# Kernel tuning notes

Hardware: AMD Instinct MI355X
Metric: run time of the kernel (lower is better)

## Reference

```python
import jax, jax.numpy as jnp
import numpy as np

DIM, H, DH = 1024, 16, 64
SCALE = 1.0 / np.sqrt(DH)


def setup_inputs() -> dict:
    key = jax.random.key(0)
    ks = jax.random.split(key, 16)
    B, S = 2, 2048
    glorot = jax.nn.initializers.glorot_uniform()
    def qkv(k):
        return glorot(k, (DIM, H, DH), jnp.float32)
    inp = {
        "x": jax.random.normal(ks[0], (B, S, DIM), jnp.float32),
        "layer_idx": 3,
        "lambda_param": jnp.full((1,), 0.8, jnp.float32),
    }
    for i, br in enumerate(["1", "2"]):
        base = 1 + i * 4
        inp[f"Wq{br}"] = qkv(ks[base])
        inp[f"Wk{br}"] = qkv(ks[base + 1])
        inp[f"Wv{br}"] = qkv(ks[base + 2])
        inp[f"Wo{br}"] = glorot(ks[base + 3], (H, DH, DIM), jnp.float32).reshape(H, DH, DIM)
        inp[f"bq{br}"] = jnp.zeros((H, DH), jnp.float32)
        inp[f"bk{br}"] = jnp.zeros((H, DH), jnp.float32)
        inp[f"bv{br}"] = jnp.zeros((H, DH), jnp.float32)
        inp[f"bo{br}"] = jnp.zeros((DIM,), jnp.float32)
    inp["Wp"] = glorot(ks[9], (DIM, DIM), jnp.float32)
    inp["bp"] = jnp.zeros((DIM,), jnp.float32)
    return inp


def _mha(x, Wq, bq, Wk, bk, Wv, bv, Wo, bo):
    # x: [B,S,D]; per-head projections as in keras.layers.MultiHeadAttention
    q = jnp.einsum("bsd,dhk->bshk", x, Wq) + bq   # [B,S,H,Dh]
    k = jnp.einsum("bsd,dhk->bshk", x, Wk) + bk
    v = jnp.einsum("bsd,dhk->bshk", x, Wv) + bv
    scores = jnp.einsum("bqhd,bkhd->bhqk", q, k) * SCALE  # [B,H,S,S]
    attn = jax.nn.softmax(scores, axis=-1)
    o = jnp.einsum("bhqk,bkhd->bqhd", attn, v)            # [B,S,H,Dh]
    return jnp.einsum("bqhd,hdo->bqo", o, Wo) + bo        # [B,S,D]


def _get_lambda(lambda_param, layer_idx):
    lf = jnp.asarray(layer_idx, jnp.float32)
    exp_term = jnp.exp(-0.3 * jnp.maximum(lf - 1.0, 0.0))
    init = 0.8 - 0.6 * exp_term
    return jnp.clip(init * lambda_param[0], 0.1, 0.9)


def reference(x, layer_idx, lambda_param,
              Wq1, bq1, Wk1, bk1, Wv1, bv1, Wo1, bo1,
              Wq2, bq2, Wk2, bk2, Wv2, bv2, Wo2, bo2,
              Wp, bp):
    a1 = _mha(x, Wq1, bq1, Wk1, bk1, Wv1, bv1, Wo1, bo1)
    a2 = _mha(x, Wq2, bq2, Wk2, bk2, Wv2, bv2, Wo2, bo2)
    lam = _get_lambda(lambda_param, layer_idx)
    diff = a1 - lam * a2
    return diff @ Wp + bp  # dropout is identity at inference
```

## Files before the change

kernel.cpp:

```cpp
#include <hip/hip_runtime.h>
#include <math.h>

typedef unsigned short u16;
typedef __attribute__((ext_vector_type(8))) short bf16x8;
typedef __attribute__((ext_vector_type(4))) float f32x4;
typedef __attribute__((ext_vector_type(4))) unsigned short u16x4;
typedef __attribute__((ext_vector_type(8))) unsigned short u16x8;

constexpr int Sq = 2048, Dm = 1024, Hh = 16, DH = 64;
constexpr int NT = 4096;
constexpr float SEXP = 0.125f * 1.44269504f;

#if __has_builtin(__builtin_amdgcn_exp2f)
#define EXP2(x) __builtin_amdgcn_exp2f(x)
#else
#define EXP2(x) exp2f(x)
#endif

__device__ __forceinline__ u16 f2bf(float f) {
    unsigned u = __float_as_uint(f);
    return (u16)((u + 0x7FFF + ((u >> 16) & 1)) >> 16);
}

__device__ __forceinline__ void async16(u16* lds, const u16* g) {
    __builtin_amdgcn_global_load_lds(
        (const __attribute__((address_space(1))) unsigned int*)g,
        (__attribute__((address_space(3))) unsigned int*)lds, 16, 0, 0);
}

__device__ __forceinline__ float lam_of(const int* lidx, const float* lamp) {
    float lf = (float)lidx[0];
    float init = 0.8f - 0.6f * __expf(-0.3f * fmaxf(lf - 1.0f, 0.0f));
    return fminf(fmaxf(init * lamp[0], 0.1f), 0.9f);
}

__device__ __forceinline__ void gemm_tile_128(
    const u16* __restrict__ A, const u16* __restrict__ Bt, int K,
    int aRow0, int bCol0, u16* As, u16* Bs, f32x4 acc[4][4])
{
    const int tid = threadIdx.x;
    const int w = tid >> 6, lane = tid & 63;
    const int ln = lane & 15, quad = lane >> 4;
    const int wm = (w >> 1) * 64, wn = (w & 1) * 64;
    const int l3 = lane & 7, lr8 = lane >> 3;

    for (int kt = 0; kt < K; kt += 64) {
        __syncthreads();
        #pragma unroll
        for (int c0 = 0; c0 < 4; ++c0) {
            int c = w * 4 + c0;
            int lr = c * 8 + lr8;
            int sc = l3 ^ (lr & 7);
            async16(As + c * 512, A + (size_t)(aRow0 + lr) * K + kt + sc * 8);
            async16(Bs + c * 512, Bt + (size_t)(bCol0 + lr) * K + kt + sc * 8);
        }
        __syncthreads();
        #pragma unroll
        for (int kc = 0; kc < 2; ++kc) {
            bf16x8 af[4], bfr[4];
            #pragma unroll
            for (int mt = 0; mt < 4; ++mt)
                af[mt] = *(const bf16x8*)(As + (wm + mt * 16 + ln) * 64 +
                                          (((kc * 4 + quad) ^ (ln & 7)) * 8));
            #pragma unroll
            for (int nt = 0; nt < 4; ++nt)
                bfr[nt] = *(const bf16x8*)(Bs + (wn + nt * 16 + ln) * 64 +
                                           (((kc * 4 + quad) ^ (ln & 7)) * 8));
            #pragma unroll
            for (int mt = 0; mt < 4; ++mt)
                #pragma unroll
                for (int nt = 0; nt < 4; ++nt)
                    acc[mt][nt] = __builtin_amdgcn_mfma_f32_16x16x32_bf16(
                        af[mt], bfr[nt], acc[mt][nt], 0, 0, 0);
        }
    }
}

__device__ __forceinline__ void gemm_tile_64(
    const u16* __restrict__ A, const u16* __restrict__ Bt, int K,
    int aRow0, int bCol0, u16* As, u16* Bs, f32x4 acc[2][4])
{
    const int tid = threadIdx.x;
    const int w = tid >> 6, lane = tid & 63;
    const int ln = lane & 15, quad = lane >> 4;
    const int wm = (w >> 1) * 32, wn = (w & 1) * 64;
    const int l3 = lane & 7, lr8 = lane >> 3;

    for (int kt = 0; kt < K; kt += 64) {
        __syncthreads();
        #pragma unroll
        for (int c0 = 0; c0 < 2; ++c0) {
            int c = w * 2 + c0;
            int lr = c * 8 + lr8;
            int sc = l3 ^ (lr & 7);
            async16(As + c * 512, A + (size_t)(aRow0 + lr) * K + kt + sc * 8);
        }
        #pragma unroll
        for (int c0 = 0; c0 < 4; ++c0) {
            int c = w * 4 + c0;
            int lr = c * 8 + lr8;
            int sc = l3 ^ (lr & 7);
            async16(Bs + c * 512, Bt + (size_t)(bCol0 + lr) * K + kt + sc * 8);
        }
        __syncthreads();
        #pragma unroll
        for (int kc = 0; kc < 2; ++kc) {
            bf16x8 af[2], bfr[4];
            #pragma unroll
            for (int mt = 0; mt < 2; ++mt)
                af[mt] = *(const bf16x8*)(As + (wm + mt * 16 + ln) * 64 +
                                          (((kc * 4 + quad) ^ (ln & 7)) * 8));
            #pragma unroll
            for (int nt = 0; nt < 4; ++nt)
                bfr[nt] = *(const bf16x8*)(Bs + (wn + nt * 16 + ln) * 64 +
                                           (((kc * 4 + quad) ^ (ln & 7)) * 8));
            #pragma unroll
            for (int mt = 0; mt < 2; ++mt)
                #pragma unroll
                for (int nt = 0; nt < 4; ++nt)
                    acc[mt][nt] = __builtin_amdgcn_mfma_f32_16x16x32_bf16(
                        af[mt], bfr[nt], acc[mt][nt], 0, 0, 0);
        }
    }
}

__global__ __launch_bounds__(256)
void convert_x(const float* __restrict__ x, u16* __restrict__ xb)
{
    int i = (blockIdx.x * 256 + threadIdx.x) * 4;
    float4 v = *(const float4*)(x + i);
    u16x4 o;
    o.x = f2bf(v.x); o.y = f2bf(v.y); o.z = f2bf(v.z); o.w = f2bf(v.w);
    *(u16x4*)(xb + i) = o;
}

struct TcP { const float* src[7]; u16* dst[7]; };

__global__ __launch_bounds__(256)
void wconv(TcP p)
{
    __shared__ float t[64][65];
    const int z = blockIdx.z;
    const float* __restrict__ src = p.src[z];
    u16* __restrict__ dst = p.dst[z];
    const int kb = blockIdx.y * 64, nb = blockIdx.x * 64;
    const int tid = threadIdx.x;
    {
        int r = tid >> 2, cs = (tid & 3) * 16;
        #pragma unroll
        for (int j4 = 0; j4 < 16; j4 += 4) {
            float4 v = *(const float4*)&src[(size_t)(kb + r) * 1024 + nb + cs + j4];
            t[r][cs + j4 + 0] = v.x; t[r][cs + j4 + 1] = v.y;
            t[r][cs + j4 + 2] = v.z; t[r][cs + j4 + 3] = v.w;
        }
    }
    __syncthreads();
    {
        int n = tid >> 2, ks = (tid & 3) * 16;
        u16x8 a, b;
        #pragma unroll
        for (int j = 0; j < 8; ++j) a[j] = f2bf(t[ks + j][n]);
        #pragma unroll
        for (int j = 0; j < 8; ++j) b[j] = f2bf(t[ks + 8 + j][n]);
        u16* o = &dst[(size_t)(nb + n) * 1024 + kb + ks];
        *(u16x8*)o = a;
        *(u16x8*)(o + 8) = b;
    }
}

__global__ __launch_bounds__(256)
void woconv(const float* __restrict__ Wo1, const float* __restrict__ Wo2,
            const float* __restrict__ bo1, const float* __restrict__ bo2,
            const int* __restrict__ lidx, const float* __restrict__ lamp,
            u16* __restrict__ Acat)
{
    const float lam = lam_of(lidx, lamp);
    int i = (blockIdx.x * 256 + threadIdx.x) * 4;
    float4 v;
    if (i < 1048576) {
        v = *(const float4*)(Wo1 + i);
    } else if (i < 2097152) {
        v = *(const float4*)(Wo2 + (i - 1048576));
        v.x *= -lam; v.y *= -lam; v.z *= -lam; v.w *= -lam;
    } else {
        int c = i - 2097152;
        float4 a = *(const float4*)(bo1 + c);
        float4 b = *(const float4*)(bo2 + c);
        v.x = a.x - lam * b.x; v.y = a.y - lam * b.y;
        v.z = a.z - lam * b.z; v.w = a.w - lam * b.w;
    }
    u16x4 o;
    o.x = f2bf(v.x); o.y = f2bf(v.y); o.z = f2bf(v.z); o.w = f2bf(v.w);
    *(u16x4*)(Acat + i) = o;
}

__global__ __launch_bounds__(256, 4)
void wfull_mfma(const u16* __restrict__ Acat, const u16* __restrict__ Wpt,
                const float* __restrict__ bp, u16* __restrict__ Wfull_bt,
                float* __restrict__ bfull)
{
    __shared__ u16 As[64 * 64], Bs[128 * 64];
    const int aRow0 = blockIdx.y * 64, nCol0 = blockIdx.x * 128;
    f32x4 acc[2][4] = {};
    gemm_tile_64(Acat, Wpt, 1024, aRow0, nCol0, As, Bs, acc);

    const int tid = threadIdx.x, w = tid >> 6, lane = tid & 63;
    const int ln = lane & 15, quad = lane >> 4;
    const int wm = (w >> 1) * 32, wn = (w & 1) * 64;
    #pragma unroll
    for (int mt = 0; mt < 2; ++mt) {
        #pragma unroll
        for (int nt = 0; nt < 4; ++nt) {
            int gn = nCol0 + wn + nt * 16 + ln;
            #pragma unroll
            for (int r = 0; r < 4; ++r) {
                int gm = aRow0 + wm + mt * 16 + quad * 4 + r;
                if (gm < 2048)
                    Wfull_bt[(size_t)gn * 2048 + gm] = f2bf(acc[mt][nt][r]);
                else if (gm == 2048)
                    bfull[gn] = acc[mt][nt][r] + bp[gn];
            }
        }
    }
}

struct QkvP { const u16* Wt[6]; const float* bias[6]; u16* out[6]; };

__global__ __launch_bounds__(256, 3)
void qkv_mfma(const u16* __restrict__ xb, QkvP p)
{
    __shared__ u16 As[128 * 64], Bs[128 * 64];
    const int z = blockIdx.z;
    const int type = (z < 3) ? z : z - 3;
    const int aRow0 = blockIdx.y * 128, nCol0 = blockIdx.x * 128;
    f32x4 acc[4][4] = {};
    gemm_tile_128(xb, p.Wt[z], 1024, aRow0, nCol0, As, Bs, acc);

    const float* __restrict__ bias = p.bias[z];
    u16* __restrict__ out = p.out[z];
    const int tid = threadIdx.x, w = tid >> 6, lane = tid & 63;
    const int ln = lane & 15, quad = lane >> 4;
    const int wm = (w >> 1) * 64, wn = (w & 1) * 64;
    #pragma unroll
    for (int mt = 0; mt < 4; ++mt) {
        #pragma unroll
        for (int nt = 0; nt < 4; ++nt) {
            int gn = nCol0 + wn + nt * 16 + ln;
            int h = gn >> 6, dh = gn & 63;
            float bv = bias[gn];
            #pragma unroll
            for (int r = 0; r < 4; ++r) {
                int gm = aRow0 + wm + mt * 16 + quad * 4 + r;
                int b = gm >> 11, s = gm & (Sq - 1);
                size_t bh = (size_t)(b * Hh + h);
                float fv = acc[mt][nt][r] + bv;
                size_t idx;
                u16 val;
                if (type == 0) {
                    val = f2bf(fv * SEXP);
                    idx = bh * 131072 + (size_t)s * 64 + dh;
                } else if (type == 1) {
                    val = f2bf(fv);
                    idx = bh * 131072 + (size_t)(s >> 5) * 2048 +
                          (size_t)((dh >> 5) * 2 + ((s >> 4) & 1)) * 512 +
                          (size_t)(((dh >> 3) & 3) * 16 + (s & 15)) * 8 + (dh & 7);
                } else {
                    val = f2bf(fv);
                    int kidx = ((s & 15) * 2) + ((s >> 4) & 1);
                    idx = bh * 131072 + (size_t)(s >> 5) * 2048 +
                          (size_t)(dh >> 4) * 512 +
                          (size_t)((kidx >> 3) * 16 + (dh & 15)) * 8 + (kidx & 7);
                }
                out[idx] = val;
            }
        }
    }
}

__global__ __launch_bounds__(256, 4)
void attn_mfma(const u16* __restrict__ q1, const u16* __restrict__ kf1,
               const u16* __restrict__ vf1,
               const u16* __restrict__ q2, const u16* __restrict__ kf2,
               const u16* __restrict__ vf2, u16* __restrict__ ocat)
{
    __shared__ __align__(16) char smem[10240];

    const int bh = blockIdx.x, qblk = blockIdx.y, br = blockIdx.z;
    const u16* __restrict__ q  = br ? q2  : q1;
    const u16* __restrict__ kf = br ? kf2 : kf1;
    const u16* __restrict__ vf = br ? vf2 : vf1;

    const int tid = threadIdx.x, w = tid >> 6, lane = tid & 63;
    const int ln = lane & 15, quad = lane >> 4;
    char* Pbase = smem + w * 2560;

    const u16* qbase = q + (size_t)bh * 131072 +
                       (size_t)(qblk * 128 + w * 32) * 64;
    bf16x8 qf[2][2];
    #pragma unroll
    for (int mt = 0; mt < 2; ++mt)
        #pragma unroll
        for (int kc = 0; kc < 2; ++kc)
            qf[mt][kc] = *(const bf16x8*)(qbase + (mt * 16 + ln) * 64 +
                                          kc * 32 + quad * 8);

    bf16x8 ones;
    #pragma unroll
    for (int j = 0; j < 8; ++j) ones[j] = (short)0x3F80;
    const f32x4 zero4 = {0.f, 0.f, 0.f, 0.f};

    f32x4 oacc[2][4] = {};
    f32x4 lacc[2] = {};

    const u16* kbase = kf + (size_t)bh * 131072 + lane * 8;
    const u16* vbase = vf + (size_t)bh * 131072 + lane * 8;

    for (int it = 0; it < 32; ++it) {
        #pragma unroll
        for (int u = 0; u < 2; ++u) {
            const int kt = it * 2 + u;
            const u16* kp = kbase + (size_t)kt * 2048;
            const u16* vp = vbase + (size_t)kt * 2048;

            bf16x8 kfr[2][2];
            #pragma unroll
            for (int kc = 0; kc < 2; ++kc)
                #pragma unroll
                for (int nt = 0; nt < 2; ++nt)
                    kfr[nt][kc] = *(const bf16x8*)(kp + (kc * 2 + nt) * 512);

            f32x4 sacc[2][2];
            #pragma unroll
            for (int mt = 0; mt < 2; ++mt)
                #pragma unroll
                for (int nt = 0; nt < 2; ++nt)
                    sacc[mt][nt] = __builtin_amdgcn_mfma_f32_16x16x32_bf16(
                        qf[mt][0], kfr[nt][0], zero4, 0, 0, 0);
            #pragma unroll
            for (int mt = 0; mt < 2; ++mt)
                #pragma unroll
                for (int nt = 0; nt < 2; ++nt)
                    sacc[mt][nt] = __builtin_amdgcn_mfma_f32_16x16x32_bf16(
                        qf[mt][1], kfr[nt][1], sacc[mt][nt], 0, 0, 0);

            #pragma unroll
            for (int mt = 0; mt < 2; ++mt) {
                #pragma unroll
                for (int r = 0; r < 4; ++r) {
                    float p0 = EXP2(sacc[mt][0][r]);
                    float p1 = EXP2(sacc[mt][1][r]);
                    unsigned a  = __float_as_uint(p0) + 0x8000u;
                    unsigned b2 = __float_as_uint(p1) + 0x8000u;
                    unsigned pk = __builtin_amdgcn_perm(b2, a, 0x07060302);
                    int row = mt * 16 + quad * 4 + r;
                    *(unsigned*)(Pbase + row * 80 + (((ln >> 2) ^ r) << 4) +
                                 ((ln & 3) << 2)) = pk;
                }
            }

            bf16x8 vfr[4];
            #pragma unroll
            for (int dt = 0; dt < 4; ++dt)
                vfr[dt] = *(const bf16x8*)(vp + dt * 512);

            #pragma unroll
            for (int mt = 0; mt < 2; ++mt) {
                bf16x8 pf = *(const bf16x8*)(Pbase + (mt * 16 + ln) * 80 +
                                             ((quad ^ (ln & 3)) << 4));
                lacc[mt] = __builtin_amdgcn_mfma_f32_16x16x32_bf16(
                    pf, ones, lacc[mt], 0, 0, 0);
                #pragma unroll
                for (int dt = 0; dt < 4; ++dt)
                    oacc[mt][dt] = __builtin_amdgcn_mfma_f32_16x16x32_bf16(
                        pf, vfr[dt], oacc[mt][dt], 0, 0, 0);
            }
        }
        __builtin_amdgcn_s_barrier();
    }

    const int b = bh >> 4, h = bh & 15;
    #pragma unroll
    for (int mt = 0; mt < 2; ++mt) {
        #pragma unroll
        for (int r = 0; r < 4; ++r) {
            float inv = 1.0f / lacc[mt][r];
            int s = qblk * 128 + w * 32 + mt * 16 + quad * 4 + r;
            size_t rowb = (size_t)(b * Sq + s) * 2048 + br * 1024 + h * 64;
            #pragma unroll
            for (int dt = 0; dt < 4; ++dt)
                ocat[rowb + dt * 16 + ln] = f2bf(oacc[mt][dt][r] * inv);
        }
    }
}

__global__ __launch_bounds__(256, 4)
void out_mfma(const u16* __restrict__ ocat, const u16* __restrict__ Wfull_bt,
              const float* __restrict__ bfull, float* __restrict__ outb)
{
    __shared__ u16 As[64 * 64], Bs[128 * 64];
    const int aRow0 = blockIdx.y * 64, nCol0 = blockIdx.x * 128;
    f32x4 acc[2][4] = {};
    gemm_tile_64(ocat, Wfull_bt, 2048, aRow0, nCol0, As, Bs, acc);

    const int tid = threadIdx.x, w = tid >> 6, lane = tid & 63;
    const int ln = lane & 15, quad = lane >> 4;
    const int wm = (w >> 1) * 32, wn = (w & 1) * 64;
    #pragma unroll
    for (int mt = 0; mt < 2; ++mt) {
        #pragma unroll
        for (int nt = 0; nt < 4; ++nt) {
            int gn = nCol0 + wn + nt * 16 + ln;
            float bv = bfull[gn];
            #pragma unroll
            for (int r = 0; r < 4; ++r) {
                int gm = aRow0 + wm + mt * 16 + quad * 4 + r;
                outb[(size_t)gm * 1024 + gn] = acc[mt][nt][r] + bv;
            }
        }
    }
}

extern "C" void kernel_launch(void* const* d_in, const int* in_sizes, int n_in,
                              void* d_out, int out_size, void* d_ws, size_t ws_size,
                              hipStream_t stream)
{
    const float* x    = (const float*)d_in[0];
    const int*   lidx = (const int*)  d_in[1];
    const float* lamp = (const float*)d_in[2];
    const float* Wq1  = (const float*)d_in[3];
    const float* Wk1  = (const float*)d_in[4];
    const float* Wv1  = (const float*)d_in[5];
    const float* Wo1  = (const float*)d_in[6];
    const float* bq1  = (const float*)d_in[7];
    const float* bk1  = (const float*)d_in[8];
    const float* bv1  = (const float*)d_in[9];
    const float* bo1  = (const float*)d_in[10];
    const float* Wq2  = (const float*)d_in[11];
    const float* Wk2  = (const float*)d_in[12];
    const float* Wv2  = (const float*)d_in[13];
    const float* Wo2  = (const float*)d_in[14];
    const float* bq2  = (const float*)d_in[15];
    const float* bk2  = (const float*)d_in[16];
    const float* bv2  = (const float*)d_in[17];
    const float* bo2  = (const float*)d_in[18];
    const float* Wp   = (const float*)d_in[19];
    const float* bp   = (const float*)d_in[20];

    char* wsb = (char*)d_ws;
    const size_t MB = 1 << 20;
    u16* xb    = (u16*)(wsb + 0 * MB);
    u16* Wt0   = (u16*)(wsb + 8 * MB);
    u16* Wpt   = (u16*)(wsb + 20 * MB);
    u16* Acat  = (u16*)(wsb + 22 * MB);
    u16* Wfull = (u16*)(wsb + 27 * MB);
    float* bfull = (float*)(wsb + 31 * MB);
    u16* qb1   = (u16*)(wsb + 32 * MB);
    u16* kb1   = (u16*)(wsb + 40 * MB);
    u16* vb1   = (u16*)(wsb + 48 * MB);
    u16* qb2   = (u16*)(wsb + 56 * MB);
    u16* kb2   = (u16*)(wsb + 64 * MB);
    u16* vb2   = (u16*)(wsb + 72 * MB);
    u16* ocat  = (u16*)(wsb + 80 * MB);

    convert_x<<<dim3(NT * Dm / 1024), dim3(256), 0, stream>>>(x, xb);

    TcP tp;
    const float* wsrc[7] = {Wq1, Wk1, Wv1, Wq2, Wk2, Wv2, Wp};
    for (int i = 0; i < 7; ++i) tp.src[i] = wsrc[i];
    for (int i = 0; i < 6; ++i) tp.dst[i] = Wt0 + (size_t)i * 1024 * 1024;
    tp.dst[6] = Wpt;
    wconv<<<dim3(16, 16, 7), dim3(256), 0, stream>>>(tp);

    woconv<<<dim3(2049), dim3(256), 0, stream>>>(
        Wo1, Wo2, bo1, bo2, lidx, lamp, Acat);

    wfull_mfma<<<dim3(8, 33), dim3(256), 0, stream>>>(
        Acat, Wpt, bp, Wfull, bfull);

    QkvP qp;
    qp.Wt[0] = Wt0 + 0 * 1048576; qp.bias[0] = bq1; qp.out[0] = qb1;
    qp.Wt[1] = Wt0 + 1 * 1048576; qp.bias[1] = bk1; qp.out[1] = kb1;
    qp.Wt[2] = Wt0 + 2 * 1048576; qp.bias[2] = bv1; qp.out[2] = vb1;
    qp.Wt[3] = Wt0 + 3 * 1048576; qp.bias[3] = bq2; qp.out[3] = qb2;
    qp.Wt[4] = Wt0 + 4 * 1048576; qp.bias[4] = bk2; qp.out[4] = kb2;
    qp.Wt[5] = Wt0 + 5 * 1048576; qp.bias[5] = bv2; qp.out[5] = vb2;
    qkv_mfma<<<dim3(8, 32, 6), dim3(256), 0, stream>>>(xb, qp);

    attn_mfma<<<dim3(32, 16, 2), dim3(256), 0, stream>>>(
        qb1, kb1, vb1, qb2, kb2, vb2, ocat);

    out_mfma<<<dim3(8, 64), dim3(256), 0, stream>>>(
        ocat, Wfull, bfull, (float*)d_out);
}
```

Measured before the change: 333.2 us.

## Widen QKV GEMM tiles to 128x256 and software-pipeline attention P buffer

The QKV projection now treats the six weight matrices as one concatenated 6144-wide B operand and uses 128x256 tiles, so each wave holds 4x8 accumulators. This halves redundant A-tile loads, at the cost of more registers and occupancy lowered to 2. The attention loop now double-buffers the per-wave P tile in LDS and software-pipelines QK^T/exp for key tile k with the PV product for tile k-1. This overlaps exp work with MFMA, but doubles LDS use and lowers the occupancy hint from 4 to 3.

```diff
diff --git a/kernel.cpp b/kernel.cpp
--- a/kernel.cpp
+++ b/kernel.cpp
@@ -32,48 +32,6 @@
     float lf = (float)lidx[0];
     float init = 0.8f - 0.6f * __expf(-0.3f * fmaxf(lf - 1.0f, 0.0f));
     return fminf(fmaxf(init * lamp[0], 0.1f), 0.9f);
-}
-
-__device__ __forceinline__ void gemm_tile_128(
-    const u16* __restrict__ A, const u16* __restrict__ Bt, int K,
-    int aRow0, int bCol0, u16* As, u16* Bs, f32x4 acc[4][4])
-{
-    const int tid = threadIdx.x;
-    const int w = tid >> 6, lane = tid & 63;
-    const int ln = lane & 15, quad = lane >> 4;
-    const int wm = (w >> 1) * 64, wn = (w & 1) * 64;
-    const int l3 = lane & 7, lr8 = lane >> 3;
-
-    for (int kt = 0; kt < K; kt += 64) {
-        __syncthreads();
-        #pragma unroll
-        for (int c0 = 0; c0 < 4; ++c0) {
-            int c = w * 4 + c0;
-            int lr = c * 8 + lr8;
-            int sc = l3 ^ (lr & 7);
-            async16(As + c * 512, A + (size_t)(aRow0 + lr) * K + kt + sc * 8);
-            async16(Bs + c * 512, Bt + (size_t)(bCol0 + lr) * K + kt + sc * 8);
-        }
-        __syncthreads();
-        #pragma unroll
-        for (int kc = 0; kc < 2; ++kc) {
-            bf16x8 af[4], bfr[4];
-            #pragma unroll
-            for (int mt = 0; mt < 4; ++mt)
-                af[mt] = *(const bf16x8*)(As + (wm + mt * 16 + ln) * 64 +
-                                          (((kc * 4 + quad) ^ (ln & 7)) * 8));
-            #pragma unroll
-            for (int nt = 0; nt < 4; ++nt)
-                bfr[nt] = *(const bf16x8*)(Bs + (wn + nt * 16 + ln) * 64 +
-                                           (((kc * 4 + quad) ^ (ln & 7)) * 8));
-            #pragma unroll
-            for (int mt = 0; mt < 4; ++mt)
-                #pragma unroll
-                for (int nt = 0; nt < 4; ++nt)
-                    acc[mt][nt] = __builtin_amdgcn_mfma_f32_16x16x32_bf16(
-                        af[mt], bfr[nt], acc[mt][nt], 0, 0, 0);
-        }
-    }
 }
 
 __device__ __forceinline__ void gemm_tile_64(
@@ -224,30 +182,71 @@
     }
 }
 
-struct QkvP { const u16* Wt[6]; const float* bias[6]; u16* out[6]; };
-
-__global__ __launch_bounds__(256, 3)
-void qkv_mfma(const u16* __restrict__ xb, QkvP p)
-{
-    __shared__ u16 As[128 * 64], Bs[128 * 64];
-    const int z = blockIdx.z;
+struct QkvP { const float* bias[6]; u16* out[6]; };
+
+__global__ __launch_bounds__(256, 2)
+void qkv_mfma(const u16* __restrict__ xb, const u16* __restrict__ Wt_all, QkvP p)
+{
+    __shared__ u16 As[128 * 64], Bs[256 * 64];
+    const int nCol0 = blockIdx.x * 256;
+    const int aRow0 = blockIdx.y * 128;
+    const int z = nCol0 >> 10;
     const int type = (z < 3) ? z : z - 3;
-    const int aRow0 = blockIdx.y * 128, nCol0 = blockIdx.x * 128;
-    f32x4 acc[4][4] = {};
-    gemm_tile_128(xb, p.Wt[z], 1024, aRow0, nCol0, As, Bs, acc);
+
+    const int tid = threadIdx.x, w = tid >> 6, lane = tid & 63;
+    const int ln = lane & 15, quad = lane >> 4;
+    const int wm = (w >> 1) * 64, wn = (w & 1) * 128;
+    const int l3 = lane & 7, lr8 = lane >> 3;
+
+    f32x4 acc[4][8] = {};
+
+    for (int kt = 0; kt < 1024; kt += 64) {
+        __syncthreads();
+        #pragma unroll
+        for (int c0 = 0; c0 < 4; ++c0) {
+            int c = w * 4 + c0;
+            int lr = c * 8 + lr8;
+            int sc = l3 ^ (lr & 7);
+            async16(As + c * 512, xb + (size_t)(aRow0 + lr) * 1024 + kt + sc * 8);
+        }
+        #pragma unroll
+        for (int c0 = 0; c0 < 8; ++c0) {
+            int c = w * 8 + c0;
+            int lr = c * 8 + lr8;
+            int sc = l3 ^ (lr & 7);
+            async16(Bs + c * 512,
+                    Wt_all + (size_t)(nCol0 + lr) * 1024 + kt + sc * 8);
+        }
+        __syncthreads();
+        #pragma unroll
+        for (int kc = 0; kc < 2; ++kc) {
+            bf16x8 af[4], bfr[8];
+            #pragma unroll
+            for (int mt = 0; mt < 4; ++mt)
+                af[mt] = *(const bf16x8*)(As + (wm + mt * 16 + ln) * 64 +
+                                          (((kc * 4 + quad) ^ (ln & 7)) * 8));
+            #pragma unroll
+            for (int nt = 0; nt < 8; ++nt)
+                bfr[nt] = *(const bf16x8*)(Bs + (wn + nt * 16 + ln) * 64 +
+                                           (((kc * 4 + quad) ^ (ln & 7)) * 8));
+            #pragma unroll
+            for (int mt = 0; mt < 4; ++mt)
+                #pragma unroll
+                for (int nt = 0; nt < 8; ++nt)
+                    acc[mt][nt] = __builtin_amdgcn_mfma_f32_16x16x32_bf16(
+                        af[mt], bfr[nt], acc[mt][nt], 0, 0, 0);
+        }
+    }
 
     const float* __restrict__ bias = p.bias[z];
     u16* __restrict__ out = p.out[z];
-    const int tid = threadIdx.x, w = tid >> 6, lane = tid & 63;
-    const int ln = lane & 15, quad = lane >> 4;
-    const int wm = (w >> 1) * 64, wn = (w & 1) * 64;
     #pragma unroll
     for (int mt = 0; mt < 4; ++mt) {
         #pragma unroll
-        for (int nt = 0; nt < 4; ++nt) {
-            int gn = nCol0 + wn + nt * 16 + ln;
-            int h = gn >> 6, dh = gn & 63;
-            float bv = bias[gn];
+        for (int nt = 0; nt < 8; ++nt) {
+            int col = (nCol0 + wn + nt * 16 + ln) & 1023;
+            int h = col >> 6, dh = col & 63;
+            float bv = bias[col];
             #pragma unroll
             for (int r = 0; r < 4; ++r) {
                 int gm = aRow0 + wm + mt * 16 + quad * 4 + r;
@@ -277,13 +276,74 @@
     }
 }
 
-__global__ __launch_bounds__(256, 4)
+__device__ __forceinline__ void attn_step(
+    int kt, const u16* kbase, const u16* vbase, char* Pw, char* Pr,
+    const bf16x8 qf[2][2], bf16x8 ones,
+    f32x4 oacc[2][4], f32x4 lacc[2], int ln, int quad)
+{
+    const f32x4 zero4 = {0.f, 0.f, 0.f, 0.f};
+    const u16* kp = kbase + (size_t)kt * 2048;
+    const u16* vp = vbase + (size_t)(kt - 1) * 2048;
+
+    bf16x8 kfr[2][2], vfr[4];
+    #pragma unroll
+    for (int kc = 0; kc < 2; ++kc)
+        #pragma unroll
+        for (int nt = 0; nt < 2; ++nt)
+            kfr[nt][kc] = *(const bf16x8*)(kp + (kc * 2 + nt) * 512);
+    #pragma unroll
+    for (int dt = 0; dt < 4; ++dt)
+        vfr[dt] = *(const bf16x8*)(vp + dt * 512);
+
+    f32x4 sacc[2][2];
+    #pragma unroll
+    for (int mt = 0; mt < 2; ++mt)
+        #pragma unroll
+        for (int nt = 0; nt < 2; ++nt)
+            sacc[mt][nt] = __builtin_amdgcn_mfma_f32_16x16x32_bf16(
+                qf[mt][0], kfr[nt][0], zero4, 0, 0, 0);
+    #pragma unroll
+    for (int mt = 0; mt < 2; ++mt)
+        #pragma unroll
+        for (int nt = 0; nt < 2; ++nt)
+            sacc[mt][nt] = __builtin_amdgcn_mfma_f32_16x16x32_bf16(
+                qf[mt][1], kfr[nt][1], sacc[mt][nt], 0, 0, 0);
+
+    #pragma unroll
+    for (int mt = 0; mt < 2; ++mt) {
+        #pragma unroll
+        for (int r = 0; r < 4; ++r) {
+            float p0 = EXP2(sacc[mt][0][r]);
+            float p1 = EXP2(sacc[mt][1][r]);
+            unsigned a  = __float_as_uint(p0) + 0x8000u;
+            unsigned b2 = __float_as_uint(p1) + 0x8000u;
+            unsigned pk = __builtin_amdgcn_perm(b2, a, 0x07060302);
+            int row = mt * 16 + quad * 4 + r;
+            *(unsigned*)(Pw + row * 80 + (((ln >> 2) ^ r) << 4) +
+                         ((ln & 3) << 2)) = pk;
+        }
+    }
+
+    #pragma unroll
+    for (int mt = 0; mt < 2; ++mt) {
+        bf16x8 pf = *(const bf16x8*)(Pr + (mt * 16 + ln) * 80 +
+                                     ((quad ^ (ln & 3)) << 4));
+        lacc[mt] = __builtin_amdgcn_mfma_f32_16x16x32_bf16(
+            pf, ones, lacc[mt], 0, 0, 0);
+        #pragma unroll
+        for (int dt = 0; dt < 4; ++dt)
+            oacc[mt][dt] = __builtin_amdgcn_mfma_f32_16x16x32_bf16(
+                pf, vfr[dt], oacc[mt][dt], 0, 0, 0);
+    }
+}
+
+__global__ __launch_bounds__(256, 3)
 void attn_mfma(const u16* __restrict__ q1, const u16* __restrict__ kf1,
                const u16* __restrict__ vf1,
                const u16* __restrict__ q2, const u16* __restrict__ kf2,
                const u16* __restrict__ vf2, u16* __restrict__ ocat)
 {
-    __shared__ __align__(16) char smem[10240];
+    __shared__ __align__(16) char smem[20480];
 
     const int bh = blockIdx.x, qblk = blockIdx.y, br = blockIdx.z;
     const u16* __restrict__ q  = br ? q2  : q1;
@@ -292,7 +352,8 @@
 
     const int tid = threadIdx.x, w = tid >> 6, lane = tid & 63;
     const int ln = lane & 15, quad = lane >> 4;
-    char* Pbase = smem + w * 2560;
+    char* P0 = smem + w * 5120;
+    char* P1 = P0 + 2560;
 
     const u16* qbase = q + (size_t)bh * 131072 +
                        (size_t)(qblk * 128 + w * 32) * 64;
@@ -315,67 +376,66 @@
     const u16* kbase = kf + (size_t)bh * 131072 + lane * 8;
     const u16* vbase = vf + (size_t)bh * 131072 + lane * 8;
 
-    for (int it = 0; it < 32; ++it) {
-        #pragma unroll
-        for (int u = 0; u < 2; ++u) {
-            const int kt = it * 2 + u;
-            const u16* kp = kbase + (size_t)kt * 2048;
-            const u16* vp = vbase + (size_t)kt * 2048;
-
-            bf16x8 kfr[2][2];
-            #pragma unroll
-            for (int kc = 0; kc < 2; ++kc)
-                #pragma unroll
-                for (int nt = 0; nt < 2; ++nt)
-                    kfr[nt][kc] = *(const bf16x8*)(kp + (kc * 2 + nt) * 512);
-
-            f32x4 sacc[2][2];
-            #pragma unroll
-            for (int mt = 0; mt < 2; ++mt)
-                #pragma unroll
-                for (int nt = 0; nt < 2; ++nt)
-                    sacc[mt][nt] = __builtin_amdgcn_mfma_f32_16x16x32_bf16(
-                        qf[mt][0], kfr[nt][0], zero4, 0, 0, 0);
-            #pragma unroll
-            for (int mt = 0; mt < 2; ++mt)
-                #pragma unroll
-                for (int nt = 0; nt < 2; ++nt)
-                    sacc[mt][nt] = __builtin_amdgcn_mfma_f32_16x16x32_bf16(
-                        qf[mt][1], kfr[nt][1], sacc[mt][nt], 0, 0, 0);
-
-            #pragma unroll
-            for (int mt = 0; mt < 2; ++mt) {
-                #pragma unroll
-                for (int r = 0; r < 4; ++r) {
-                    float p0 = EXP2(sacc[mt][0][r]);
-                    float p1 = EXP2(sacc[mt][1][r]);
-                    unsigned a  = __float_as_uint(p0) + 0x8000u;
-                    unsigned b2 = __float_as_uint(p1) + 0x8000u;
-                    unsigned pk = __builtin_amdgcn_perm(b2, a, 0x07060302);
-                    int row = mt * 16 + quad * 4 + r;
-                    *(unsigned*)(Pbase + row * 80 + (((ln >> 2) ^ r) << 4) +
-                                 ((ln & 3) << 2)) = pk;
-                }
+    {
+        bf16x8 kfr[2][2];
+        #pragma unroll
+        for (int kc = 0; kc < 2; ++kc)
+            #pragma unroll
+            for (int nt = 0; nt < 2; ++nt)
+                kfr[nt][kc] = *(const bf16x8*)(kbase + (kc * 2 + nt) * 512);
+        f32x4 sacc[2][2];
+        #pragma unroll
+        for (int mt = 0; mt < 2; ++mt)
+            #pragma unroll
+            for (int nt = 0; nt < 2; ++nt)
+                sacc[mt][nt] = __builtin_amdgcn_mfma_f32_16x16x32_bf16(
+                    qf[mt][0], kfr[nt][0], zero4, 0, 0, 0);
+        #pragma unroll
+        for (int mt = 0; mt < 2; ++mt)
+            #pragma unroll
+            for (int nt = 0; nt < 2; ++nt)
+                sacc[mt][nt] = __builtin_amdgcn_mfma_f32_16x16x32_bf16(
+                    qf[mt][1], kfr[nt][1], sacc[mt][nt], 0, 0, 0);
+        #pragma unroll
+        for (int mt = 0; mt < 2; ++mt) {
+            #pragma unroll
+            for (int r = 0; r < 4; ++r) {
+                float p0 = EXP2(sacc[mt][0][r]);
+                float p1 = EXP2(sacc[mt][1][r]);
+                unsigned a  = __float_as_uint(p0) + 0x8000u;
+                unsigned b2 = __float_as_uint(p1) + 0x8000u;
+                unsigned pk = __builtin_amdgcn_perm(b2, a, 0x07060302);
+                int row = mt * 16 + quad * 4 + r;
+                *(unsigned*)(P0 + row * 80 + (((ln >> 2) ^ r) << 4) +
+                             ((ln & 3) << 2)) = pk;
             }
-
-            bf16x8 vfr[4];
+        }
+    }
+
+    for (int it = 0; it < 31; ++it) {
+        attn_step(2 * it + 1, kbase, vbase, P1, P0, qf, ones, oacc, lacc, ln, quad);
+        attn_step(2 * it + 2, kbase, vbase, P0, P1, qf, ones, oacc, lacc, ln, quad);
+        __builtin_amdgcn_s_barrier();
+    }
+    attn_step(63, kbase, vbase, P1, P0, qf, ones, oacc, lacc, ln, quad);
+
+    {
+        const u16* vp = vbase + (size_t)63 * 2048;
+        bf16x8 vfr[4];
+        #pragma unroll
+        for (int dt = 0; dt < 4; ++dt)
+            vfr[dt] = *(const bf16x8*)(vp + dt * 512);
+        #pragma unroll
+        for (int mt = 0; mt < 2; ++mt) {
+            bf16x8 pf = *(const bf16x8*)(P1 + (mt * 16 + ln) * 80 +
+                                         ((quad ^ (ln & 3)) << 4));
+            lacc[mt] = __builtin_amdgcn_mfma_f32_16x16x32_bf16(
+                pf, ones, lacc[mt], 0, 0, 0);
             #pragma unroll
             for (int dt = 0; dt < 4; ++dt)
-                vfr[dt] = *(const bf16x8*)(vp + dt * 512);
-
-            #pragma unroll
-            for (int mt = 0; mt < 2; ++mt) {
-                bf16x8 pf = *(const bf16x8*)(Pbase + (mt * 16 + ln) * 80 +
-                                             ((quad ^ (ln & 3)) << 4));
-                lacc[mt] = __builtin_amdgcn_mfma_f32_16x16x32_bf16(
-                    pf, ones, lacc[mt], 0, 0, 0);
-                #pragma unroll
-                for (int dt = 0; dt < 4; ++dt)
-                    oacc[mt][dt] = __builtin_amdgcn_mfma_f32_16x16x32_bf16(
-                        pf, vfr[dt], oacc[mt][dt], 0, 0, 0);
-            }
-        }
-        __builtin_amdgcn_s_barrier();
+                oacc[mt][dt] = __builtin_amdgcn_mfma_f32_16x16x32_bf16(
+                    pf, vfr[dt], oacc[mt][dt], 0, 0, 0);
+        }
     }
 
     const int b = bh >> 4, h = bh & 15;
@@ -467,7 +527,7 @@
     TcP tp;
     const float* wsrc[7] = {Wq1, Wk1, Wv1, Wq2, Wk2, Wv2, Wp};
     for (int i = 0; i < 7; ++i) tp.src[i] = wsrc[i];
-    for (int i = 0; i < 6; ++i) tp.dst[i] = Wt0 + (size_t)i * 1024 * 1024;
+    for (int i = 0; i < 6; ++i) tp.dst[i] = Wt0 + (size_t)i * 1048576;
     tp.dst[6] = Wpt;
     wconv<<<dim3(16, 16, 7), dim3(256), 0, stream>>>(tp);
 
@@ -478,13 +538,13 @@
         Acat, Wpt, bp, Wfull, bfull);
 
     QkvP qp;
-    qp.Wt[0] = Wt0 + 0 * 1048576; qp.bias[0] = bq1; qp.out[0] = qb1;
-    qp.Wt[1] = Wt0 + 1 * 1048576; qp.bias[1] = bk1; qp.out[1] = kb1;
-    qp.Wt[2] = Wt0 + 2 * 1048576; qp.bias[2] = bv1; qp.out[2] = vb1;
-    qp.Wt[3] = Wt0 + 3 * 1048576; qp.bias[3] = bq2; qp.out[3] = qb2;
-    qp.Wt[4] = Wt0 + 4 * 1048576; qp.bias[4] = bk2; qp.out[4] = kb2;
-    qp.Wt[5] = Wt0 + 5 * 1048576; qp.bias[5] = bv2; qp.out[5] = vb2;
-    qkv_mfma<<<dim3(8, 32, 6), dim3(256), 0, stream>>>(xb, qp);
+    qp.bias[0] = bq1; qp.out[0] = qb1;
+    qp.bias[1] = bk1; qp.out[1] = kb1;
+    qp.bias[2] = bv1; qp.out[2] = vb1;
+    qp.bias[3] = bq2; qp.out[3] = qb2;
+    qp.bias[4] = bk2; qp.out[4] = kb2;
+    qp.bias[5] = bv2; qp.out[5] = vb2;
+    qkv_mfma<<<dim3(24, 32), dim3(256), 0, stream>>>(xb, Wt0, qp);
 
     attn_mfma<<<dim3(32, 16, 2), dim3(256), 0, stream>>>(
         qb1, kb1, vb1, qb2, kb2, vb2, ocat);
```

After: 342.7 us. 2.9% more time.
